# Kernel optimization log

Measured on AMD Instinct MI355X. Metric: run time of the kernel, lower is better.

Reference implementation:

```python
import jax, jax.numpy as jnp
import numpy as np

B, H, W, N = 8, 384, 384, 96
STEPSZ = 0.1; ALPHA = 0.01; BETA = 0.01; STD = 1.0
NSTEPS = 50; NSTEPS_W = 10; DMAX = 15.0; EXTGRADFAC = 10.0

def make_gauss_edge_fltr(std):
    # Gaussian-derivative edge filters, one per spatial dim: [2,1,k,k]
    r = int(np.ceil(3 * std)); t = np.arange(-r, r + 1, dtype=np.float32)
    g = np.exp(-t * t / (2 * std * std)); g /= g.sum()
    dg = -t / (std * std) * np.exp(-t * t / (2 * std * std)); dg /= np.abs(dg).sum()
    fy = np.outer(dg, g)   # d/drow
    fx = np.outer(g, dg)   # d/dcol
    return np.stack([fy, fx])[:, None].astype(np.float32)

def setup_inputs() -> dict:
    key = jax.random.key(0)
    k1, k2 = jax.random.split(key, 2)
    pred_dmap = jax.random.normal(k1, (B, 1, H, W), jnp.float32)
    nodes = jax.random.uniform(k2, (B, N, 2), jnp.float32)
    nodes = nodes * jnp.array([H - 1.0, W - 1.0], jnp.float32)
    nodes = jnp.sort(nodes, axis=1)  # roughly monotone chain -> path-like snake
    widths = jnp.ones((B, N), jnp.float32) * 3.0
    fltr = jnp.asarray(make_gauss_edge_fltr(STD))
    return {"pred_dmap": pred_dmap, "nodes": nodes, "widths": widths, "fltr": fltr}

def grad_im(x, fltr):
    # x: [B,1,H,W], fltr: [2,1,k,k] -> [B,2,H,W]
    return jax.lax.conv_general_dilated(x, fltr, (1, 1), 'SAME',
                                        dimension_numbers=('NCHW', 'OIHW', 'NCHW'))

def interp(img, pts):
    # bilinear sample: img [C,H,W], pts [N,2] (row,col) -> [N,C]
    C, Hh, Ww = img.shape
    y = jnp.clip(pts[:, 0], 0.0, Hh - 1.0); x = jnp.clip(pts[:, 1], 0.0, Ww - 1.0)
    y0 = jnp.floor(y).astype(jnp.int32); x0 = jnp.floor(x).astype(jnp.int32)
    y1 = jnp.minimum(y0 + 1, Hh - 1); x1 = jnp.minimum(x0 + 1, Ww - 1)
    wy = y - y0; wx = x - x0
    v00 = img[:, y0, x0]; v01 = img[:, y0, x1]
    v10 = img[:, y1, x0]; v11 = img[:, y1, x1]
    v = v00 * (1 - wy) * (1 - wx) + v01 * (1 - wy) * wx + v10 * wy * (1 - wx) + v11 * wy * wx
    return v.T

def d2_open(x):
    # second difference with replicated endpoints (open snake)
    xp = jnp.concatenate([x[:1], x, x[-1:]], 0)
    return xp[:-2] - 2 * xp[1:-1] + xp[2:]

def snake_one(nodes, widths, g, gw):
    # explicit active-contour iterations on node positions
    def pstep(x, _):
        fext = interp(g, x)                       # [N,2] external force
        d2 = d2_open(x); d4 = d2_open(d2)
        return x + STEPSZ * (ALPHA * d2 - BETA * d4 + fext), None
    x, _ = jax.lax.scan(pstep, nodes, None, length=NSTEPS)
    # unit normals from central-difference tangents
    t = jnp.concatenate([x[1:2] - x[0:1], 0.5 * (x[2:] - x[:-2]), x[-1:] - x[-2:-1]], 0)
    n = jnp.stack([-t[:, 1], t[:, 0]], 1)
    n = n / (jnp.linalg.norm(n, axis=1, keepdims=True) + 1e-6)
    def wstep(w, _):
        gp = interp(gw, x + w[:, None] * n); gm = interp(gw, x - w[:, None] * n)
        f = 0.5 * (jnp.sum(gp * n, 1) - jnp.sum(gm * n, 1))
        return jnp.maximum(w + STEPSZ * f, 0.5), None
    w, _ = jax.lax.scan(wstep, widths, None, length=NSTEPS_W)
    return x, w

def render(x, w):
    # distance-to-ribbon map, clipped at DMAX; only [HW,S] intermediates
    ys, xs = jnp.meshgrid(jnp.arange(H, dtype=jnp.float32),
                          jnp.arange(W, dtype=jnp.float32), indexing='ij')
    P = jnp.stack([ys.ravel(), xs.ravel()], 1)          # [HW,2]
    a = x[:-1]; ab = x[1:] - a                          # [S,2]
    denom = jnp.sum(ab * ab, 1) + 1e-8                  # [S]
    dotpa = P @ ab.T - jnp.sum(a * ab, 1)               # [HW,S] = (P-a).ab
    t = jnp.clip(dotpa / denom, 0.0, 1.0)
    pa2 = jnp.sum(P * P, 1)[:, None] - 2 * (P @ a.T) + jnp.sum(a * a, 1)  # |P-a|^2
    d = jnp.sqrt(jnp.maximum(pa2 - 2 * t * dotpa + t * t * denom, 0.0))
    ws = 0.5 * (w[:-1] + w[1:])                         # per-segment width
    dmap = jnp.min(jnp.maximum(d - ws, 0.0), axis=1)
    return jnp.minimum(dmap, DMAX).reshape(H, W)

def reference(pred_dmap, nodes, widths, fltr):
    gimg = grad_im(pred_dmap, fltr) * EXTGRADFAC          # [B,2,H,W]
    gimgW = grad_im(jnp.abs(pred_dmap), fltr) * EXTGRADFAC
    def per_sample(nd, wd, g, gw):
        x, w = snake_one(nd, wd, g, gw)
        return render(x, w)
    dm = jax.vmap(per_sample)(nodes, widths, gimg, gimgW)[:, None]  # [B,1,H,W]
    dm = jax.lax.stop_gradient(dm)   # snake_dm.detach() in the original
    return jnp.mean((pred_dmap - dm) ** 2)
```

## Files before the change

### kernel.cpp

```cpp
#include <hip/hip_runtime.h>
#include <math.h>

#define BB   8
#define HH   384
#define WW   384
#define NN   96
#define HWSZ (HH * WW)
#define NSEG (NN - 1)
#define SEGF 12
#define DMAXV 15.0f
#define ROWS_PER_BLK 12
#define NCHUNK (HH / ROWS_PER_BLK)
#define CROWS 12
#define CBANDS (HH / CROWS)

__device__ inline void load_taps(const float* __restrict__ fltr,
                                 float* __restrict__ sg, float* __restrict__ sdg)
{
    int tid = threadIdx.x;
    if (tid < 7) {
        float s = 0.f;
#pragma unroll
        for (int i = 0; i < 7; ++i) s += fabsf(fltr[i * 7 + tid]);
        sg[tid] = s;
    } else if (tid < 14) {
        int r = tid - 7;
        float s = 0.f;
#pragma unroll
        for (int j = 0; j < 7; ++j) s += fltr[r * 7 + j];
        sdg[r] = s;
    }
    __syncthreads();
}

__global__ __launch_bounds__(384) void conv_fused(
    const float* __restrict__ pred, const float* __restrict__ fltr,
    float2* __restrict__ g2, float2* __restrict__ gw2,
    float* __restrict__ accum, unsigned int* __restrict__ counter)
{
    __shared__ float sg[7], sdg[7];
    load_taps(fltr, sg, sdg);
    if (blockIdx.x == 0 && threadIdx.x == 0) {
        atomicExch(accum, 0.0f);
        atomicExch(counter, 0u);
    }

    int blk = blockIdx.x;
    int b = blk & 7;
    int band = blk >> 3;
    int y0 = band * CROWS;
    int x = threadIdx.x;
    const float* pb = pred + (size_t)b * HWSZ;
    bool xin = (x >= 3) && (x < WW - 3);

    float hg[7], hd[7], hga[7], hda[7];

#pragma unroll
    for (int q = 0; q < CROWS + 6; ++q) {
        float vg = 0.f, vd = 0.f, vga = 0.f, vda = 0.f;
        int r = y0 + q - 3;
        if (r >= 0 && r < HH) {
            const float* row = pb + r * WW;
            if (xin) {
#pragma unroll
                for (int k = 0; k < 7; ++k) {
                    float v  = row[x + k - 3];
                    float av = fabsf(v);
                    vg  = fmaf(v,  sg[k],  vg);
                    vd  = fmaf(v,  sdg[k], vd);
                    vga = fmaf(av, sg[k],  vga);
                    vda = fmaf(av, sdg[k], vda);
                }
            } else {
#pragma unroll
                for (int k = 0; k < 7; ++k) {
                    int ix = x + k - 3;
                    float v  = (ix >= 0 && ix < WW) ? row[ix] : 0.f;
                    float av = fabsf(v);
                    vg  = fmaf(v,  sg[k],  vg);
                    vd  = fmaf(v,  sdg[k], vd);
                    vga = fmaf(av, sg[k],  vga);
                    vda = fmaf(av, sdg[k], vda);
                }
            }
        }
        hg[q % 7] = vg; hd[q % 7] = vd; hga[q % 7] = vga; hda[q % 7] = vda;

        if (q >= 6) {
            int y = y0 + q - 6;
            float o0 = 0.f, o1 = 0.f, o2 = 0.f, o3 = 0.f;
#pragma unroll
            for (int j = 0; j < 7; ++j) {
                int s = (q - 6 + j) % 7;
                o0 = fmaf(hg[s],  sdg[j], o0);
                o1 = fmaf(hd[s],  sg[j],  o1);
                o2 = fmaf(hga[s], sdg[j], o2);
                o3 = fmaf(hda[s], sg[j],  o3);
            }
            size_t gi = (size_t)b * HWSZ + (size_t)y * WW + x;
            g2[gi]  = make_float2(o0 * 10.f, o1 * 10.f);
            gw2[gi] = make_float2(o2 * 10.f, o3 * 10.f);
        }
    }
}

__device__ inline float2 bilin2i(const float2* __restrict__ img, float py, float px)
{
    float y = fminf(fmaxf(py, 0.0f), (float)(HH - 1));
    float x = fminf(fmaxf(px, 0.0f), (float)(WW - 1));
    int y0 = (int)floorf(y);
    int x0 = (int)floorf(x);
    int y1 = min(y0 + 1, HH - 1);
    bool xedge = (x0 + 1 > WW - 1);
    float wy = y - (float)y0;
    float wx = x - (float)x0;
    float4 r0 = *(const float4*)(img + y0 * WW + x0);
    float4 r1 = *(const float4*)(img + y1 * WW + x0);
    float2 v00 = make_float2(r0.x, r0.y);
    float2 v01 = xedge ? v00 : make_float2(r0.z, r0.w);
    float2 v10 = make_float2(r1.x, r1.y);
    float2 v11 = xedge ? v10 : make_float2(r1.z, r1.w);
    float w00 = (1.f - wy) * (1.f - wx);
    float w01 = (1.f - wy) * wx;
    float w10 = wy * (1.f - wx);
    float w11 = wy * wx;
    return make_float2(v00.x * w00 + v01.x * w01 + v10.x * w10 + v11.x * w11,
                       v00.y * w00 + v01.y * w01 + v10.y * w10 + v11.y * w11);
}

__device__ inline void write_seg(float* __restrict__ r,
                                 float py, float px, float qy, float qx, float wseg)
{
    float aby = qy - py, abx = qx - px;
    float denom = aby * aby + abx * abx + 1e-8f;
    float aab = py * aby + px * abx;
    float aa  = py * py + px * px;
    float reach = DMAXV + wseg;
    r[0]  = py;   r[1]  = px;
    r[2]  = aby;  r[3]  = abx;
    r[4]  = aab;  r[5]  = denom;
    r[6]  = 1.0f / denom;
    r[7]  = aa;   r[8]  = wseg;
    r[9]  = fminf(py, qy) - reach;
    r[10] = fmaxf(py, qy) + reach;
    r[11] = 0.f;
}

__global__ __launch_bounds__(64) void snake_kernel(
    const float* __restrict__ nodes, const float* __restrict__ widths,
    const float* __restrict__ g2, const float* __restrict__ gw2,
    float* __restrict__ segs)
{
    int b = blockIdx.x;
    int t = threadIdx.x;

    const float2* gb  = (const float2*)g2  + (size_t)b * HWSZ;
    const float2* gwb = (const float2*)gw2 + (size_t)b * HWSZ;
    const int HALF = NN / 2;
    bool act = (t < HALF);
    bool t0 = (t == 0), tl = (t == HALF - 1);

    float ay = 0.f, ax = 0.f, by = 0.f, bx = 0.f;
    if (act) {
        float4 n4 = *(const float4*)(nodes + (size_t)(b * NN + 2 * t) * 2);
        ay = n4.x; ax = n4.y; by = n4.z; bx = n4.w;
    }

    for (int s = 0; s < 50; ++s) {
        float2 fa = bilin2i(gb, ay, ax);
        float2 fb = bilin2i(gb, by, bx);

        float aLy = __shfl_up(ay, 1, 64),  aLx = __shfl_up(ax, 1, 64);
        float bLy = __shfl_up(by, 1, 64),  bLx = __shfl_up(bx, 1, 64);
        float aRy = __shfl_down(ay, 1, 64), aRx = __shfl_down(ax, 1, 64);
        float bRy = __shfl_down(by, 1, 64), bRx = __shfl_down(bx, 1, 64);
        bLy = t0 ? ay : bLy;  bLx = t0 ? ax : bLx;
        aRy = tl ? by : aRy;  aRx = tl ? bx : aRx;

        float d2m_y = aLy - 2.f * bLy + ay;
        float d2a_y = bLy - 2.f * ay + by;
        float d2b_y = ay  - 2.f * by + aRy;
        float d2p_y = by  - 2.f * aRy + bRy;
        d2m_y = t0 ? d2a_y : d2m_y;
        d2p_y = tl ? d2b_y : d2p_y;
        float d4a_y = d2m_y - 2.f * d2a_y + d2b_y;
        float d4b_y = d2a_y - 2.f * d2b_y + d2p_y;

        float d2m_x = aLx - 2.f * bLx + ax;
        float d2a_x = bLx - 2.f * ax + bx;
        float d2b_x = ax  - 2.f * bx + aRx;
        float d2p_x = bx  - 2.f * aRx + bRx;
        d2m_x = t0 ? d2a_x : d2m_x;
        d2p_x = tl ? d2b_x : d2p_x;
        float d4a_x = d2m_x - 2.f * d2a_x + d2b_x;
        float d4b_x = d2a_x - 2.f * d2b_x + d2p_x;

        ay += 0.1f * (0.01f * d2a_y - 0.01f * d4a_y + fa.x);
        ax += 0.1f * (0.01f * d2a_x - 0.01f * d4a_x + fa.y);
        by += 0.1f * (0.01f * d2b_y - 0.01f * d4b_y + fb.x);
        bx += 0.1f * (0.01f * d2b_x - 0.01f * d4b_x + fb.y);
    }

    {
        float bLy = __shfl_up(by, 1, 64), bLx = __shfl_up(bx, 1, 64);
        float aRy = __shfl_down(ay, 1, 64), aRx = __shfl_down(ax, 1, 64);
        float tay = 0.5f * (by - bLy), tax = 0.5f * (bx - bLx);
        if (t0) { tay = by - ay; tax = bx - ax; }
        float tby = 0.5f * (aRy - ay), tbx = 0.5f * (aRx - ax);
        if (tl) { tby = by - ay; tbx = bx - ax; }

        float na0 = -tax, na1 = tay;
        float nrm = sqrtf(na0 * na0 + na1 * na1) + 1e-6f;
        float nay = na0 / nrm, nax = na1 / nrm;
        float nb0 = -tbx, nb1 = tby;
        nrm = sqrtf(nb0 * nb0 + nb1 * nb1) + 1e-6f;
        float nby = nb0 / nrm, nbx = nb1 / nrm;

        float wa = 0.f, wb = 0.f;
        if (act) { wa = widths[b * NN + 2 * t]; wb = widths[b * NN + 2 * t + 1]; }
        for (int s = 0; s < 10; ++s) {
            float2 pa = bilin2i(gwb, ay + wa * nay, ax + wa * nax);
            float2 ma = bilin2i(gwb, ay - wa * nay, ax - wa * nax);
            float2 pb = bilin2i(gwb, by + wb * nby, bx + wb * nbx);
            float2 mb = bilin2i(gwb, by - wb * nby, bx - wb * nbx);
            float fa = 0.5f * ((pa.x * nay + pa.y * nax) - (ma.x * nay + ma.y * nax));
            float fb = 0.5f * ((pb.x * nby + pb.y * nbx) - (mb.x * nby + mb.y * nbx));
            wa = fmaxf(wa + 0.1f * fa, 0.5f);
            wb = fmaxf(wb + 0.1f * fb, 0.5f);
        }

        float aRy2 = __shfl_down(ay, 1, 64), aRx2 = __shfl_down(ax, 1, 64);
        float waR  = __shfl_down(wa, 1, 64);
        if (act) {
            float* r0 = segs + (size_t)(b * NSEG + 2 * t) * SEGF;
            write_seg(r0, ay, ax, by, bx, 0.5f * (wa + wb));
            if (t < HALF - 1) {
                float* r1 = segs + (size_t)(b * NSEG + 2 * t + 1) * SEGF;
                write_seg(r1, by, bx, aRy2, aRx2, 0.5f * (wb + waR));
            }
        }
    }
}

__global__ __launch_bounds__(384) void render_kernel(
    const float* __restrict__ pred, const float* __restrict__ segs,
    float* __restrict__ accum, unsigned int* __restrict__ counter,
    float* __restrict__ out)
{
    __shared__ float ss[NSEG * SEGF];
    __shared__ int slo, shi;
    __shared__ float swsum[6];

    int blk = blockIdx.x;
    int b = blk & 7;
    int chunk = blk >> 3;
    int y0 = chunk * ROWS_PER_BLK;
    int t = threadIdx.x;

    const float* sb = segs + (size_t)b * NSEG * SEGF;
    for (int j = t; j < NSEG * SEGF; j += 384) ss[j] = sb[j];
    if (t == 0) { slo = NSEG; shi = -1; }
    __syncthreads();

    float cy0 = (float)y0, cy1 = (float)(y0 + ROWS_PER_BLK - 1);
    if (t < NSEG) {
        float ylo = ss[t * SEGF + 9];
        float yhi = ss[t * SEGF + 10];
        if (yhi >= cy0 && ylo <= cy1) {
            atomicMin(&slo, t);
            atomicMax(&shi, t);
        }
    }
    __syncthreads();
    int lo = slo, hi = shi;

    float px = (float)t;
    float px2 = px * px;
    float minv[ROWS_PER_BLK];
#pragma unroll
    for (int r = 0; r < ROWS_PER_BLK; ++r) minv[r] = DMAXV;

    for (int si = lo; si <= hi; ++si) {
        const float* r = ss + si * SEGF;
        float ay = r[0], ax = r[1], aby = r[2], abx = r[3];
        float aab = r[4], denom = r[5], invd = r[6], aa = r[7], ws = r[8];
        float dotpa_b = fmaf(px, abx, -aab);
        float pa2_b   = fmaf(px, -2.0f * ax, px2 + aa);
#pragma unroll
        for (int ry = 0; ry < ROWS_PER_BLK; ++ry) {
            float py = (float)(y0 + ry);
            float dotpa = fmaf(py, aby, dotpa_b);
            float tt = fminf(fmaxf(dotpa * invd, 0.0f), 1.0f);
            float pa2 = fmaf(py, fmaf(py, 1.0f, -2.0f * ay), pa2_b);
            float d2 = fmaf(tt, fmaf(tt, denom, -2.0f * dotpa), pa2);
            float d = sqrtf(fmaxf(d2, 0.0f));
            float v = fmaxf(d - ws, 0.0f);
            minv[ry] = fminf(minv[ry], v);
        }
    }

    const float* pb = pred + (size_t)b * HWSZ + (size_t)y0 * WW + t;
    float sq = 0.f;
#pragma unroll
    for (int ry = 0; ry < ROWS_PER_BLK; ++ry) {
        float diff = pb[ry * WW] - minv[ry];
        sq = fmaf(diff, diff, sq);
    }

#pragma unroll
    for (int off = 32; off > 0; off >>= 1) sq += __shfl_down(sq, off, 64);
    if ((t & 63) == 0) swsum[t >> 6] = sq;
    __syncthreads();
    if (t == 0) {
        float tot = swsum[0] + swsum[1] + swsum[2] + swsum[3] + swsum[4] + swsum[5];
        atomicAdd(accum, tot);
        __threadfence();
        unsigned int done = atomicAdd(counter, 1u);
        if (done == (unsigned int)(BB * NCHUNK - 1)) {
            float total = atomicAdd(accum, 0.0f);
            out[0] = total * (1.0f / (float)(BB * HWSZ));
        }
    }
}

extern "C" void kernel_launch(void* const* d_in, const int* in_sizes, int n_in,
                              void* d_out, int out_size, void* d_ws, size_t ws_size,
                              hipStream_t stream)
{
    const float* pred   = (const float*)d_in[0];
    const float* nodes  = (const float*)d_in[1];
    const float* widths = (const float*)d_in[2];
    const float* fltr   = (const float*)d_in[3];
    float* out = (float*)d_out;

    float* ws   = (float*)d_ws;
    float* g2   = ws;
    float* gw2  = g2 + (size_t)2 * BB * HWSZ;
    float* segs = gw2 + (size_t)2 * BB * HWSZ;
    float* accum = segs + (size_t)BB * NSEG * SEGF;
    unsigned int* counter = (unsigned int*)(accum + 1);

    conv_fused<<<BB * CBANDS, 384, 0, stream>>>(pred, fltr, (float2*)g2, (float2*)gw2,
                                                accum, counter);
    snake_kernel<<<BB, 64, 0, stream>>>(nodes, widths, g2, gw2, segs);
    render_kernel<<<BB * NCHUNK, 384, 0, stream>>>(pred, segs, accum, counter, out);
}
```

Measured before the change: 135.4 us.

## Fuse conv, snake and render into one persistent kernel with flag sync

Merges the three kernels (gradient convolution, snake iteration, distance-map render) into a single launch of 256 blocks. Blocks coordinate through global atomic counters: per-batch conv completion counts gate the snake blocks, and a per-batch flag gates the render phase. The final reduction writes per-block partials that the last block sums in a fixed order. This removes two kernel launch gaps and the drain between stages. It relies on all 256 blocks being co-resident, or the spin-waits could deadlock, and render blocks sit idle while the single-wave snake runs.

```diff
diff --git a/kernel.cpp b/kernel.cpp
--- a/kernel.cpp
+++ b/kernel.cpp
@@ -9,8 +9,6 @@
 #define NSEG (NN - 1)
 #define SEGF 12
 #define DMAXV 15.0f
-#define ROWS_PER_BLK 12
-#define NCHUNK (HH / ROWS_PER_BLK)
 #define CROWS 12
 #define CBANDS (HH / CROWS)
 
@@ -31,77 +29,6 @@
         sdg[r] = s;
     }
     __syncthreads();
-}
-
-__global__ __launch_bounds__(384) void conv_fused(
-    const float* __restrict__ pred, const float* __restrict__ fltr,
-    float2* __restrict__ g2, float2* __restrict__ gw2,
-    float* __restrict__ accum, unsigned int* __restrict__ counter)
-{
-    __shared__ float sg[7], sdg[7];
-    load_taps(fltr, sg, sdg);
-    if (blockIdx.x == 0 && threadIdx.x == 0) {
-        atomicExch(accum, 0.0f);
-        atomicExch(counter, 0u);
-    }
-
-    int blk = blockIdx.x;
-    int b = blk & 7;
-    int band = blk >> 3;
-    int y0 = band * CROWS;
-    int x = threadIdx.x;
-    const float* pb = pred + (size_t)b * HWSZ;
-    bool xin = (x >= 3) && (x < WW - 3);
-
-    float hg[7], hd[7], hga[7], hda[7];
-
-#pragma unroll
-    for (int q = 0; q < CROWS + 6; ++q) {
-        float vg = 0.f, vd = 0.f, vga = 0.f, vda = 0.f;
-        int r = y0 + q - 3;
-        if (r >= 0 && r < HH) {
-            const float* row = pb + r * WW;
-            if (xin) {
-#pragma unroll
-                for (int k = 0; k < 7; ++k) {
-                    float v  = row[x + k - 3];
-                    float av = fabsf(v);
-                    vg  = fmaf(v,  sg[k],  vg);
-                    vd  = fmaf(v,  sdg[k], vd);
-                    vga = fmaf(av, sg[k],  vga);
-                    vda = fmaf(av, sdg[k], vda);
-                }
-            } else {
-#pragma unroll
-                for (int k = 0; k < 7; ++k) {
-                    int ix = x + k - 3;
-                    float v  = (ix >= 0 && ix < WW) ? row[ix] : 0.f;
-                    float av = fabsf(v);
-                    vg  = fmaf(v,  sg[k],  vg);
-                    vd  = fmaf(v,  sdg[k], vd);
-                    vga = fmaf(av, sg[k],  vga);
-                    vda = fmaf(av, sdg[k], vda);
-                }
-            }
-        }
-        hg[q % 7] = vg; hd[q % 7] = vd; hga[q % 7] = vga; hda[q % 7] = vda;
-
-        if (q >= 6) {
-            int y = y0 + q - 6;
-            float o0 = 0.f, o1 = 0.f, o2 = 0.f, o3 = 0.f;
-#pragma unroll
-            for (int j = 0; j < 7; ++j) {
-                int s = (q - 6 + j) % 7;
-                o0 = fmaf(hg[s],  sdg[j], o0);
-                o1 = fmaf(hd[s],  sg[j],  o1);
-                o2 = fmaf(hga[s], sdg[j], o2);
-                o3 = fmaf(hda[s], sg[j],  o3);
-            }
-            size_t gi = (size_t)b * HWSZ + (size_t)y * WW + x;
-            g2[gi]  = make_float2(o0 * 10.f, o1 * 10.f);
-            gw2[gi] = make_float2(o2 * 10.f, o3 * 10.f);
-        }
-    }
 }
 
 __device__ inline float2 bilin2i(const float2* __restrict__ img, float py, float px)
@@ -146,179 +73,268 @@
     r[11] = 0.f;
 }
 
-__global__ __launch_bounds__(64) void snake_kernel(
+__global__ __launch_bounds__(64) void init_kernel(unsigned int* __restrict__ flags)
+{
+    if (threadIdx.x < 17) flags[threadIdx.x] = 0u;
+}
+
+__global__ __launch_bounds__(384) void fused_kernel(
+    const float* __restrict__ pred, const float* __restrict__ fltr,
     const float* __restrict__ nodes, const float* __restrict__ widths,
-    const float* __restrict__ g2, const float* __restrict__ gw2,
-    float* __restrict__ segs)
-{
-    int b = blockIdx.x;
-    int t = threadIdx.x;
-
-    const float2* gb  = (const float2*)g2  + (size_t)b * HWSZ;
-    const float2* gwb = (const float2*)gw2 + (size_t)b * HWSZ;
-    const int HALF = NN / 2;
-    bool act = (t < HALF);
-    bool t0 = (t == 0), tl = (t == HALF - 1);
-
-    float ay = 0.f, ax = 0.f, by = 0.f, bx = 0.f;
-    if (act) {
-        float4 n4 = *(const float4*)(nodes + (size_t)(b * NN + 2 * t) * 2);
-        ay = n4.x; ax = n4.y; by = n4.z; bx = n4.w;
-    }
-
-    for (int s = 0; s < 50; ++s) {
-        float2 fa = bilin2i(gb, ay, ax);
-        float2 fb = bilin2i(gb, by, bx);
-
-        float aLy = __shfl_up(ay, 1, 64),  aLx = __shfl_up(ax, 1, 64);
-        float bLy = __shfl_up(by, 1, 64),  bLx = __shfl_up(bx, 1, 64);
-        float aRy = __shfl_down(ay, 1, 64), aRx = __shfl_down(ax, 1, 64);
-        float bRy = __shfl_down(by, 1, 64), bRx = __shfl_down(bx, 1, 64);
-        bLy = t0 ? ay : bLy;  bLx = t0 ? ax : bLx;
-        aRy = tl ? by : aRy;  aRx = tl ? bx : aRx;
-
-        float d2m_y = aLy - 2.f * bLy + ay;
-        float d2a_y = bLy - 2.f * ay + by;
-        float d2b_y = ay  - 2.f * by + aRy;
-        float d2p_y = by  - 2.f * aRy + bRy;
-        d2m_y = t0 ? d2a_y : d2m_y;
-        d2p_y = tl ? d2b_y : d2p_y;
-        float d4a_y = d2m_y - 2.f * d2a_y + d2b_y;
-        float d4b_y = d2a_y - 2.f * d2b_y + d2p_y;
-
-        float d2m_x = aLx - 2.f * bLx + ax;
-        float d2a_x = bLx - 2.f * ax + bx;
-        float d2b_x = ax  - 2.f * bx + aRx;
-        float d2p_x = bx  - 2.f * aRx + bRx;
-        d2m_x = t0 ? d2a_x : d2m_x;
-        d2p_x = tl ? d2b_x : d2p_x;
-        float d4a_x = d2m_x - 2.f * d2a_x + d2b_x;
-        float d4b_x = d2a_x - 2.f * d2b_x + d2p_x;
-
-        ay += 0.1f * (0.01f * d2a_y - 0.01f * d4a_y + fa.x);
-        ax += 0.1f * (0.01f * d2a_x - 0.01f * d4a_x + fa.y);
-        by += 0.1f * (0.01f * d2b_y - 0.01f * d4b_y + fb.x);
-        bx += 0.1f * (0.01f * d2b_x - 0.01f * d4b_x + fb.y);
-    }
-
-    {
-        float bLy = __shfl_up(by, 1, 64), bLx = __shfl_up(bx, 1, 64);
-        float aRy = __shfl_down(ay, 1, 64), aRx = __shfl_down(ax, 1, 64);
-        float tay = 0.5f * (by - bLy), tax = 0.5f * (bx - bLx);
-        if (t0) { tay = by - ay; tax = bx - ax; }
-        float tby = 0.5f * (aRy - ay), tbx = 0.5f * (aRx - ax);
-        if (tl) { tby = by - ay; tbx = bx - ax; }
-
-        float na0 = -tax, na1 = tay;
-        float nrm = sqrtf(na0 * na0 + na1 * na1) + 1e-6f;
-        float nay = na0 / nrm, nax = na1 / nrm;
-        float nb0 = -tbx, nb1 = tby;
-        nrm = sqrtf(nb0 * nb0 + nb1 * nb1) + 1e-6f;
-        float nby = nb0 / nrm, nbx = nb1 / nrm;
-
-        float wa = 0.f, wb = 0.f;
-        if (act) { wa = widths[b * NN + 2 * t]; wb = widths[b * NN + 2 * t + 1]; }
-        for (int s = 0; s < 10; ++s) {
-            float2 pa = bilin2i(gwb, ay + wa * nay, ax + wa * nax);
-            float2 ma = bilin2i(gwb, ay - wa * nay, ax - wa * nax);
-            float2 pb = bilin2i(gwb, by + wb * nby, bx + wb * nbx);
-            float2 mb = bilin2i(gwb, by - wb * nby, bx - wb * nbx);
-            float fa = 0.5f * ((pa.x * nay + pa.y * nax) - (ma.x * nay + ma.y * nax));
-            float fb = 0.5f * ((pb.x * nby + pb.y * nbx) - (mb.x * nby + mb.y * nbx));
-            wa = fmaxf(wa + 0.1f * fa, 0.5f);
-            wb = fmaxf(wb + 0.1f * fb, 0.5f);
-        }
-
-        float aRy2 = __shfl_down(ay, 1, 64), aRx2 = __shfl_down(ax, 1, 64);
-        float waR  = __shfl_down(wa, 1, 64);
-        if (act) {
-            float* r0 = segs + (size_t)(b * NSEG + 2 * t) * SEGF;
-            write_seg(r0, ay, ax, by, bx, 0.5f * (wa + wb));
-            if (t < HALF - 1) {
-                float* r1 = segs + (size_t)(b * NSEG + 2 * t + 1) * SEGF;
-                write_seg(r1, by, bx, aRy2, aRx2, 0.5f * (wb + waR));
-            }
-        }
-    }
-}
-
-__global__ __launch_bounds__(384) void render_kernel(
-    const float* __restrict__ pred, const float* __restrict__ segs,
-    float* __restrict__ accum, unsigned int* __restrict__ counter,
-    float* __restrict__ out)
-{
+    float2* __restrict__ g2, float2* __restrict__ gw2,
+    float* __restrict__ segs, float* __restrict__ partials,
+    unsigned int* __restrict__ flags, float* __restrict__ out)
+{
+    __shared__ float sg[7], sdg[7];
     __shared__ float ss[NSEG * SEGF];
     __shared__ int slo, shi;
     __shared__ float swsum[6];
 
+    unsigned int* conv_done = flags;
+    unsigned int* seg_done  = flags + 8;
+    unsigned int* rcount    = flags + 16;
+
+    load_taps(fltr, sg, sdg);
+
     int blk = blockIdx.x;
     int b = blk & 7;
-    int chunk = blk >> 3;
-    int y0 = chunk * ROWS_PER_BLK;
-    int t = threadIdx.x;
-
-    const float* sb = segs + (size_t)b * NSEG * SEGF;
-    for (int j = t; j < NSEG * SEGF; j += 384) ss[j] = sb[j];
-    if (t == 0) { slo = NSEG; shi = -1; }
+    int band = blk >> 3;
+    int y0 = band * CROWS;
+    int tid = threadIdx.x;
+
+    {
+        int x = tid;
+        const float* pb = pred + (size_t)b * HWSZ;
+        bool xin = (x >= 3) && (x < WW - 3);
+        float hg[7], hd[7], hga[7], hda[7];
+
+#pragma unroll
+        for (int q = 0; q < CROWS + 6; ++q) {
+            float vg = 0.f, vd = 0.f, vga = 0.f, vda = 0.f;
+            int r = y0 + q - 3;
+            if (r >= 0 && r < HH) {
+                const float* row = pb + r * WW;
+                if (xin) {
+#pragma unroll
+                    for (int k = 0; k < 7; ++k) {
+                        float v  = row[x + k - 3];
+                        float av = fabsf(v);
+                        vg  = fmaf(v,  sg[k],  vg);
+                        vd  = fmaf(v,  sdg[k], vd);
+                        vga = fmaf(av, sg[k],  vga);
+                        vda = fmaf(av, sdg[k], vda);
+                    }
+                } else {
+#pragma unroll
+                    for (int k = 0; k < 7; ++k) {
+                        int ix = x + k - 3;
+                        float v  = (ix >= 0 && ix < WW) ? row[ix] : 0.f;
+                        float av = fabsf(v);
+                        vg  = fmaf(v,  sg[k],  vg);
+                        vd  = fmaf(v,  sdg[k], vd);
+                        vga = fmaf(av, sg[k],  vga);
+                        vda = fmaf(av, sdg[k], vda);
+                    }
+                }
+            }
+            hg[q % 7] = vg; hd[q % 7] = vd; hga[q % 7] = vga; hda[q % 7] = vda;
+
+            if (q >= 6) {
+                int y = y0 + q - 6;
+                float o0 = 0.f, o1 = 0.f, o2 = 0.f, o3 = 0.f;
+#pragma unroll
+                for (int j = 0; j < 7; ++j) {
+                    int s = (q - 6 + j) % 7;
+                    o0 = fmaf(hg[s],  sdg[j], o0);
+                    o1 = fmaf(hd[s],  sg[j],  o1);
+                    o2 = fmaf(hga[s], sdg[j], o2);
+                    o3 = fmaf(hda[s], sg[j],  o3);
+                }
+                size_t gi = (size_t)b * HWSZ + (size_t)y * WW + x;
+                g2[gi]  = make_float2(o0 * 10.f, o1 * 10.f);
+                gw2[gi] = make_float2(o2 * 10.f, o3 * 10.f);
+            }
+        }
+    }
+    __threadfence();
     __syncthreads();
-
-    float cy0 = (float)y0, cy1 = (float)(y0 + ROWS_PER_BLK - 1);
-    if (t < NSEG) {
-        float ylo = ss[t * SEGF + 9];
-        float yhi = ss[t * SEGF + 10];
-        if (yhi >= cy0 && ylo <= cy1) {
-            atomicMin(&slo, t);
-            atomicMax(&shi, t);
-        }
+    if (tid == 0) atomicAdd(&conv_done[b], 1u);
+
+    if (blk < 8) {
+        if (tid == 0) {
+            while (atomicAdd(&conv_done[b], 0u) < (unsigned)CBANDS)
+                __builtin_amdgcn_s_sleep(8);
+        }
+        __syncthreads();
+        __threadfence();
+
+        if (tid < 64) {
+            int t = tid;
+            const float2* gb  = g2  + (size_t)b * HWSZ;
+            const float2* gwb = gw2 + (size_t)b * HWSZ;
+            const int HALF = NN / 2;
+            bool act = (t < HALF);
+            bool t0 = (t == 0), tl = (t == HALF - 1);
+
+            float ay = 0.f, ax = 0.f, by = 0.f, bx = 0.f;
+            if (act) {
+                float4 n4 = *(const float4*)(nodes + (size_t)(b * NN + 2 * t) * 2);
+                ay = n4.x; ax = n4.y; by = n4.z; bx = n4.w;
+            }
+
+            for (int s = 0; s < 50; ++s) {
+                float2 fa = bilin2i(gb, ay, ax);
+                float2 fb = bilin2i(gb, by, bx);
+
+                float aLy = __shfl_up(ay, 1, 64),  aLx = __shfl_up(ax, 1, 64);
+                float bLy = __shfl_up(by, 1, 64),  bLx = __shfl_up(bx, 1, 64);
+                float aRy = __shfl_down(ay, 1, 64), aRx = __shfl_down(ax, 1, 64);
+                float bRy = __shfl_down(by, 1, 64), bRx = __shfl_down(bx, 1, 64);
+                bLy = t0 ? ay : bLy;  bLx = t0 ? ax : bLx;
+                aRy = tl ? by : aRy;  aRx = tl ? bx : aRx;
+
+                float d2m_y = aLy - 2.f * bLy + ay;
+                float d2a_y = bLy - 2.f * ay + by;
+                float d2b_y = ay  - 2.f * by + aRy;
+                float d2p_y = by  - 2.f * aRy + bRy;
+                d2m_y = t0 ? d2a_y : d2m_y;
+                d2p_y = tl ? d2b_y : d2p_y;
+                float d4a_y = d2m_y - 2.f * d2a_y + d2b_y;
+                float d4b_y = d2a_y - 2.f * d2b_y + d2p_y;
+
+                float d2m_x = aLx - 2.f * bLx + ax;
+                float d2a_x = bLx - 2.f * ax + bx;
+                float d2b_x = ax  - 2.f * bx + aRx;
+                float d2p_x = bx  - 2.f * aRx + bRx;
+                d2m_x = t0 ? d2a_x : d2m_x;
+                d2p_x = tl ? d2b_x : d2p_x;
+                float d4a_x = d2m_x - 2.f * d2a_x + d2b_x;
+                float d4b_x = d2a_x - 2.f * d2b_x + d2p_x;
+
+                ay += 0.1f * (0.01f * d2a_y - 0.01f * d4a_y + fa.x);
+                ax += 0.1f * (0.01f * d2a_x - 0.01f * d4a_x + fa.y);
+                by += 0.1f * (0.01f * d2b_y - 0.01f * d4b_y + fb.x);
+                bx += 0.1f * (0.01f * d2b_x - 0.01f * d4b_x + fb.y);
+            }
+
+            float bLy = __shfl_up(by, 1, 64), bLx = __shfl_up(bx, 1, 64);
+            float aRy = __shfl_down(ay, 1, 64), aRx = __shfl_down(ax, 1, 64);
+            float tay = 0.5f * (by - bLy), tax = 0.5f * (bx - bLx);
+            if (t0) { tay = by - ay; tax = bx - ax; }
+            float tby = 0.5f * (aRy - ay), tbx = 0.5f * (aRx - ax);
+            if (tl) { tby = by - ay; tbx = bx - ax; }
+
+            float na0 = -tax, na1 = tay;
+            float nrm = sqrtf(na0 * na0 + na1 * na1) + 1e-6f;
+            float nay = na0 / nrm, nax = na1 / nrm;
+            float nb0 = -tbx, nb1 = tby;
+            nrm = sqrtf(nb0 * nb0 + nb1 * nb1) + 1e-6f;
+            float nby = nb0 / nrm, nbx = nb1 / nrm;
+
+            float wa = 0.f, wb = 0.f;
+            if (act) { wa = widths[b * NN + 2 * t]; wb = widths[b * NN + 2 * t + 1]; }
+            for (int s = 0; s < 10; ++s) {
+                float2 pa = bilin2i(gwb, ay + wa * nay, ax + wa * nax);
+                float2 ma = bilin2i(gwb, ay - wa * nay, ax - wa * nax);
+                float2 pb2 = bilin2i(gwb, by + wb * nby, bx + wb * nbx);
+                float2 mb = bilin2i(gwb, by - wb * nby, bx - wb * nbx);
+                float fa = 0.5f * ((pa.x * nay + pa.y * nax) - (ma.x * nay + ma.y * nax));
+                float fb = 0.5f * ((pb2.x * nby + pb2.y * nbx) - (mb.x * nby + mb.y * nbx));
+                wa = fmaxf(wa + 0.1f * fa, 0.5f);
+                wb = fmaxf(wb + 0.1f * fb, 0.5f);
+            }
+
+            float aRy2 = __shfl_down(ay, 1, 64), aRx2 = __shfl_down(ax, 1, 64);
+            float waR  = __shfl_down(wa, 1, 64);
+            if (act) {
+                float* r0 = segs + (size_t)(b * NSEG + 2 * t) * SEGF;
+                write_seg(r0, ay, ax, by, bx, 0.5f * (wa + wb));
+                if (t < HALF - 1) {
+                    float* r1 = segs + (size_t)(b * NSEG + 2 * t + 1) * SEGF;
+                    write_seg(r1, by, bx, aRy2, aRx2, 0.5f * (wb + waR));
+                }
+            }
+        }
+        __syncthreads();
+        if (tid == 0) {
+            __threadfence();
+            atomicExch(&seg_done[b], 1u);
+        }
+    }
+
+    if (tid == 0) {
+        while (atomicAdd(&seg_done[b], 0u) == 0u)
+            __builtin_amdgcn_s_sleep(8);
     }
     __syncthreads();
-    int lo = slo, hi = shi;
-
-    float px = (float)t;
-    float px2 = px * px;
-    float minv[ROWS_PER_BLK];
-#pragma unroll
-    for (int r = 0; r < ROWS_PER_BLK; ++r) minv[r] = DMAXV;
-
-    for (int si = lo; si <= hi; ++si) {
-        const float* r = ss + si * SEGF;
-        float ay = r[0], ax = r[1], aby = r[2], abx = r[3];
-        float aab = r[4], denom = r[5], invd = r[6], aa = r[7], ws = r[8];
-        float dotpa_b = fmaf(px, abx, -aab);
-        float pa2_b   = fmaf(px, -2.0f * ax, px2 + aa);
-#pragma unroll
-        for (int ry = 0; ry < ROWS_PER_BLK; ++ry) {
-            float py = (float)(y0 + ry);
-            float dotpa = fmaf(py, aby, dotpa_b);
-            float tt = fminf(fmaxf(dotpa * invd, 0.0f), 1.0f);
-            float pa2 = fmaf(py, fmaf(py, 1.0f, -2.0f * ay), pa2_b);
-            float d2 = fmaf(tt, fmaf(tt, denom, -2.0f * dotpa), pa2);
-            float d = sqrtf(fmaxf(d2, 0.0f));
-            float v = fmaxf(d - ws, 0.0f);
-            minv[ry] = fminf(minv[ry], v);
-        }
-    }
-
-    const float* pb = pred + (size_t)b * HWSZ + (size_t)y0 * WW + t;
-    float sq = 0.f;
-#pragma unroll
-    for (int ry = 0; ry < ROWS_PER_BLK; ++ry) {
-        float diff = pb[ry * WW] - minv[ry];
-        sq = fmaf(diff, diff, sq);
-    }
-
-#pragma unroll
-    for (int off = 32; off > 0; off >>= 1) sq += __shfl_down(sq, off, 64);
-    if ((t & 63) == 0) swsum[t >> 6] = sq;
-    __syncthreads();
-    if (t == 0) {
-        float tot = swsum[0] + swsum[1] + swsum[2] + swsum[3] + swsum[4] + swsum[5];
-        atomicAdd(accum, tot);
-        __threadfence();
-        unsigned int done = atomicAdd(counter, 1u);
-        if (done == (unsigned int)(BB * NCHUNK - 1)) {
-            float total = atomicAdd(accum, 0.0f);
-            out[0] = total * (1.0f / (float)(BB * HWSZ));
+    __threadfence();
+
+    {
+        const float* sb = segs + (size_t)b * NSEG * SEGF;
+        for (int j = tid; j < NSEG * SEGF; j += 384) ss[j] = sb[j];
+        if (tid == 0) { slo = NSEG; shi = -1; }
+        __syncthreads();
+
+        float cy0 = (float)y0, cy1 = (float)(y0 + CROWS - 1);
+        if (tid < NSEG) {
+            float ylo = ss[tid * SEGF + 9];
+            float yhi = ss[tid * SEGF + 10];
+            if (yhi >= cy0 && ylo <= cy1) {
+                atomicMin(&slo, tid);
+                atomicMax(&shi, tid);
+            }
+        }
+        __syncthreads();
+        int lo = slo, hi = shi;
+
+        float px = (float)tid;
+        float px2 = px * px;
+        float minv[CROWS];
+#pragma unroll
+        for (int r = 0; r < CROWS; ++r) minv[r] = DMAXV;
+
+        for (int si = lo; si <= hi; ++si) {
+            const float* r = ss + si * SEGF;
+            float ay = r[0], ax = r[1], aby = r[2], abx = r[3];
+            float aab = r[4], denom = r[5], invd = r[6], aa = r[7], ws = r[8];
+            float dotpa_b = fmaf(px, abx, -aab);
+            float pa2_b   = fmaf(px, -2.0f * ax, px2 + aa);
+#pragma unroll
+            for (int ry = 0; ry < CROWS; ++ry) {
+                float py = (float)(y0 + ry);
+                float dotpa = fmaf(py, aby, dotpa_b);
+                float tt = fminf(fmaxf(dotpa * invd, 0.0f), 1.0f);
+                float pa2 = fmaf(py, fmaf(py, 1.0f, -2.0f * ay), pa2_b);
+                float d2 = fmaf(tt, fmaf(tt, denom, -2.0f * dotpa), pa2);
+                float d = sqrtf(fmaxf(d2, 0.0f));
+                float v = fmaxf(d - ws, 0.0f);
+                minv[ry] = fminf(minv[ry], v);
+            }
+        }
+
+        const float* pb = pred + (size_t)b * HWSZ + (size_t)y0 * WW + tid;
+        float sq = 0.f;
+#pragma unroll
+        for (int ry = 0; ry < CROWS; ++ry) {
+            float diff = pb[ry * WW] - minv[ry];
+            sq = fmaf(diff, diff, sq);
+        }
+
+#pragma unroll
+        for (int off = 32; off > 0; off >>= 1) sq += __shfl_down(sq, off, 64);
+        if ((tid & 63) == 0) swsum[tid >> 6] = sq;
+        __syncthreads();
+        if (tid == 0) {
+            float tot = swsum[0] + swsum[1] + swsum[2] + swsum[3] + swsum[4] + swsum[5];
+            partials[blk] = tot;
+            __threadfence();
+            unsigned int done = atomicAdd(rcount, 1u);
+            if (done == (unsigned int)(BB * CBANDS - 1)) {
+                __threadfence();
+                float s = 0.f;
+                for (int i = 0; i < BB * CBANDS; ++i) s += partials[i];
+                out[0] = s * (1.0f / (float)(BB * HWSZ));
+            }
         }
     }
 }
@@ -333,15 +349,15 @@
     const float* fltr   = (const float*)d_in[3];
     float* out = (float*)d_out;
 
-    float* ws   = (float*)d_ws;
-    float* g2   = ws;
-    float* gw2  = g2 + (size_t)2 * BB * HWSZ;
-    float* segs = gw2 + (size_t)2 * BB * HWSZ;
-    float* accum = segs + (size_t)BB * NSEG * SEGF;
-    unsigned int* counter = (unsigned int*)(accum + 1);
-
-    conv_fused<<<BB * CBANDS, 384, 0, stream>>>(pred, fltr, (float2*)g2, (float2*)gw2,
-                                                accum, counter);
-    snake_kernel<<<BB, 64, 0, stream>>>(nodes, widths, g2, gw2, segs);
-    render_kernel<<<BB * NCHUNK, 384, 0, stream>>>(pred, segs, accum, counter, out);
-}
+    float* ws    = (float*)d_ws;
+    float* g2    = ws;
+    float* gw2   = g2 + (size_t)2 * BB * HWSZ;
+    float* segs  = gw2 + (size_t)2 * BB * HWSZ;
+    float* partials = segs + (size_t)BB * NSEG * SEGF;
+    unsigned int* flags = (unsigned int*)(partials + BB * CBANDS);
+
+    init_kernel<<<1, 64, 0, stream>>>(flags);
+    fused_kernel<<<BB * CBANDS, 384, 0, stream>>>(
+        pred, fltr, nodes, widths, (float2*)g2, (float2*)gw2,
+        segs, partials, flags, out);
+}
```

Result: slower. 207.5 us (+53.2%).
